# Kernel optimization log

Measured on AMD Instinct MI355X. Metric: run time of the kernel, lower is better.

The kernel has to match this reference:

```python
import jax, jax.numpy as jnp
import numpy as np

NEMBEDS = 512
EMBED_DIM = 64


def setup_inputs() -> dict:
    key = jax.random.key(0)
    k1, k2 = jax.random.split(key)
    z_e = jax.random.normal(k1, (32, EMBED_DIM, 64, 64), dtype=jnp.float32)
    codebook = jax.random.uniform(
        k2, (NEMBEDS, EMBED_DIM), dtype=jnp.float32,
        minval=-1.0 / NEMBEDS, maxval=1.0 / NEMBEDS)
    return {"z_e": z_e, "codebook": codebook}


def reference(z_e, codebook):
    # NCHW -> NHWC, flatten spatial+batch into tokens
    z = jnp.transpose(z_e, (0, 2, 3, 1))          # [B,H,W,D]
    B, H, W, D = z.shape
    flat = z.reshape(-1, D)                        # [N,D]
    # squared L2 distances (argmin of ||.||_2 == argmin of ||.||_2^2)
    # expanded form avoids the [N,K,D] broadcast intermediate
    d2 = (jnp.sum(flat * flat, axis=-1, keepdims=True)
          - 2.0 * flat @ codebook.T
          + jnp.sum(codebook * codebook, axis=-1))  # [N,K]
    inds = jnp.argmin(d2, axis=1)                   # [N]
    # direct gather == one-hot matmul lookup
    z_q = codebook[inds].reshape(B, H, W, D)        # [B,H,W,D]
    # commitment + codebook loss, per-batch mean over H,W,D
    sg = jax.lax.stop_gradient
    vq_loss = (jnp.mean((sg(z) - z_q) ** 2, axis=(1, 2, 3))
               + 0.25 * jnp.mean((z - sg(z_q)) ** 2, axis=(1, 2, 3)))  # [B]
    # straight-through estimator
    z_q_st = z + sg(z_q - z)
    out = jnp.transpose(z_q_st, (0, 3, 1, 2))       # back to NCHW
    return out, vq_loss, inds[:, None]
```

## Files before the change

kernel.cpp:

```cpp
#include <hip/hip_runtime.h>

#define NEMB 512
#define DIM 64
#define NB 32
#define HW 4096
#define NTOK (NB * HW)
#define TPB 512
#define TOKBLK 512
#define BLOCKS (NTOK / TOKBLK)

typedef float f32x16 __attribute__((ext_vector_type(16)));
typedef short bf16x8 __attribute__((ext_vector_type(8)));

__device__ __forceinline__ unsigned short f2bf(float f) {
    unsigned u = __float_as_uint(f);
    unsigned r = u + 0x7FFFu + ((u >> 16) & 1u);
    return (unsigned short)(r >> 16);
}
__device__ __forceinline__ float bf2f(unsigned short h) {
    return __uint_as_float((unsigned)h << 16);
}

__global__ void vq_prep(const float* __restrict__ cb, float* __restrict__ sumc)
{
    int k = blockIdx.x * 256 + threadIdx.x;
    if (k < NEMB) {
#pragma clang fp contract(off)
        float s = 0.f;
#pragma unroll
        for (int d = 0; d < DIM; ++d) {
            float v = cb[k * DIM + d];
            float p = v * v;
            s = s + p;
        }
        sumc[k] = s;
    }
}

__global__ __launch_bounds__(TPB, 4)
void vq_main(const float* __restrict__ z_e, const float* __restrict__ cb,
             const float* __restrict__ sumc, float* __restrict__ out,
             float* __restrict__ loss_part, float* __restrict__ inds_out)
{
    __shared__ uint4 ch_s[NEMB * 9];
    __shared__ float sumc_s[NEMB];
    __shared__ float red_s[TPB];

    const int tid  = threadIdx.x;
    const int gid  = blockIdx.x;
    const int b    = gid >> 3;
    const int base = (gid & 7) * TOKBLK;
    const int w    = tid >> 6;
    const int l    = tid & 63;
    const int col  = l & 31;
    const int half = l >> 5;

    float cmax_l = 0.f;
    {
        const float4* cbg = (const float4*)cb;
#pragma unroll
        for (int i = 0; i < 8; ++i) {
            int idx = i * TPB + tid;
            int c = idx >> 3, bd = idx & 7;
            float4 v0 = cbg[idx * 2];
            float4 v1 = cbg[idx * 2 + 1];
            float vv[8] = {v0.x, v0.y, v0.z, v0.w, v1.x, v1.y, v1.z, v1.w};
            unsigned wd[4];
#pragma unroll
            for (int q = 0; q < 4; ++q) {
                cmax_l = fmaxf(cmax_l, fmaxf(fabsf(vv[2 * q]), fabsf(vv[2 * q + 1])));
                wd[q] = (unsigned)f2bf(vv[2 * q]) | ((unsigned)f2bf(vv[2 * q + 1]) << 16);
            }
            int slot = (bd + c) & 7;
            ch_s[c * 9 + slot] = make_uint4(wd[0], wd[1], wd[2], wd[3]);
        }
    }
    const float sc_v = sumc[tid];
    sumc_s[tid] = sc_v;

    const float* zb = z_e + (size_t)b * DIM * HW;
    const int t0 = base + w * 64;
    uint4 bzh[2][4], bzl[2][4];
    float l1p[2] = {0.f, 0.f}, szp[2] = {0.f, 0.f};
#pragma unroll
    for (int tt = 0; tt < 2; ++tt) {
        int tok = t0 + tt * 32 + col;
#pragma unroll
        for (int ks = 0; ks < 4; ++ks) {
            unsigned hh[8], ll[8];
#pragma unroll
            for (int j = 0; j < 8; ++j) {
                int d = 16 * ks + 8 * half + j;
                float v = zb[(size_t)d * HW + tok];
                l1p[tt] += fabsf(v);
                szp[tt] = fmaf(v, v, szp[tt]);
                unsigned short h = f2bf(v);
                unsigned short lo = f2bf(v - bf2f(h));
                hh[j] = h; ll[j] = lo;
            }
            bzh[tt][ks] = make_uint4(hh[0] | (hh[1] << 16), hh[2] | (hh[3] << 16),
                                     hh[4] | (hh[5] << 16), hh[6] | (hh[7] << 16));
            bzl[tt][ks] = make_uint4(ll[0] | (ll[1] << 16), ll[2] | (ll[3] << 16),
                                     ll[4] | (ll[5] << 16), ll[6] | (ll[7] << 16));
        }
    }
    float L1[2], SZ[2];
#pragma unroll
    for (int tt = 0; tt < 2; ++tt) {
        L1[tt] = l1p[tt] + __shfl_xor(l1p[tt], 32);
        SZ[tt] = szp[tt] + __shfl_xor(szp[tt], 32);
    }

    {
        float cm = cmax_l, sm = sc_v;
#pragma unroll
        for (int off = 32; off; off >>= 1) {
            cm = fmaxf(cm, __shfl_xor(cm, off));
            sm = fmaxf(sm, __shfl_xor(sm, off));
        }
        if (l == 0) { red_s[w] = cm; red_s[8 + w] = sm; }
    }
    __syncthreads();
    float cmax = red_s[0], scmax = red_s[8];
#pragma unroll
    for (int i = 1; i < 8; ++i) {
        cmax  = fmaxf(cmax,  red_s[i]);
        scmax = fmaxf(scmax, red_s[8 + i]);
    }

    float gapd[2];
#pragma unroll
    for (int tt = 0; tt < 2; ++tt)
        gapd[tt] = 8.0e-3f * cmax * L1[tt] + 0.5f * scmax + 1.2e-7f * SZ[tt] + 1e-6f;

    unsigned mask0[8], mask1[8];
#pragma unroll
    for (int i = 0; i < 8; ++i) { mask0[i] = 0u; mask1[i] = 0u; }
    float runm[2] = {-3.402823466e38f, -3.402823466e38f};

    for (int ct = 0; ct < 16; ++ct) {
        bf16x8 ah[4];
        const int c = 32 * ct + col;
        const int rowb = c * 9;
#pragma unroll
        for (int ks = 0; ks < 4; ++ks) {
            int slot = ((2 * ks + half) + c) & 7;
            uint4 u1 = ch_s[rowb + slot];
            ah[ks] = *(bf16x8*)&u1;
        }
#pragma unroll
        for (int tt = 0; tt < 2; ++tt) {
            f32x16 acc = {0.f, 0.f, 0.f, 0.f, 0.f, 0.f, 0.f, 0.f,
                          0.f, 0.f, 0.f, 0.f, 0.f, 0.f, 0.f, 0.f};
#pragma unroll
            for (int ks = 0; ks < 4; ++ks)
                acc = __builtin_amdgcn_mfma_f32_32x32x16_bf16(ah[ks], *(bf16x8*)&bzh[tt][ks], acc, 0, 0, 0);
#pragma unroll
            for (int ks = 0; ks < 4; ++ks)
                acc = __builtin_amdgcn_mfma_f32_32x32x16_bf16(ah[ks], *(bf16x8*)&bzl[tt][ks], acc, 0, 0, 0);
            float m = acc[0];
#pragma unroll
            for (int r = 1; r < 16; ++r) m = fmaxf(m, acc[r]);
            float rm = fmaxf(tt == 0 ? runm[0] : runm[1], m);
            if (tt == 0) runm[0] = rm; else runm[1] = rm;
            float thr = rm - (tt == 0 ? gapd[0] : gapd[1]);
            unsigned bits = 0;
#pragma unroll
            for (int r = 0; r < 16; ++r)
                bits |= (acc[r] >= thr) ? (1u << r) : 0u;
            unsigned sh = bits << ((ct & 1) * 16);
            if (tt == 0) mask0[ct >> 1] |= sh; else mask1[ct >> 1] |= sh;
        }
    }

    unsigned om[8], xm[8];
#pragma unroll
    for (int i = 0; i < 8; ++i) {
        om[i] = half ? mask1[i] : mask0[i];
        xm[i] = __shfl_xor(half ? mask0[i] : mask1[i], 32);
    }

    const int hwme = base + tid;
    float z[DIM];
    float sumz;
    {
#pragma clang fp contract(off)
        sumz = 0.f;
#pragma unroll
        for (int d = 0; d < DIM; ++d) {
            float v = zb[(size_t)d * HW + hwme];
            z[d] = v;
            float p = v * v;
            sumz = sumz + p;
        }
    }

    float best = 3.402823466e38f;
    int bk = 0;
    for (int ct = 0; ct < 16; ++ct) {
        unsigned A = (om[ct >> 1] >> ((ct & 1) * 16)) & 0xFFFFu;
        unsigned B = (xm[ct >> 1] >> ((ct & 1) * 16)) & 0xFFFFu;
        unsigned wo = ((A & 0xFu)) | (((A >> 4) & 0xFu) << 8) |
                      (((A >> 8) & 0xFu) << 16) | (((A >> 12) & 0xFu) << 24);
        unsigned wx = ((B & 0xFu)) | (((B >> 4) & 0xFu) << 8) |
                      (((B >> 8) & 0xFu) << 16) | (((B >> 12) & 0xFu) << 24);
        unsigned wc = half ? ((wo << 4) | wx) : (wo | (wx << 4));
        while (wc) {
            int kk = __builtin_ctz(wc);
            wc &= wc - 1;
            int k = 32 * ct + kk;
            const float4* c4 = (const float4*)(cb + (size_t)k * DIM);
            float a0 = 0.f;
#pragma unroll
            for (int g = 0; g < DIM / 4; ++g) {
                float4 u = c4[g];
                a0 = fmaf(z[4 * g + 0], u.x, a0);
                a0 = fmaf(z[4 * g + 1], u.y, a0);
                a0 = fmaf(z[4 * g + 2], u.z, a0);
                a0 = fmaf(z[4 * g + 3], u.w, a0);
            }
            float d2 = (sumz - 2.0f * a0) + sumc_s[k];
            if (d2 < best) { best = d2; bk = k; }
        }
    }

    inds_out[(size_t)gid * TOKBLK + tid] = (float)bk;
    float* ob = out + (size_t)b * DIM * HW;
    float lsum = 0.f;
    const float4* q4 = (const float4*)(cb + (size_t)bk * DIM);
    {
#pragma clang fp contract(off)
#pragma unroll
        for (int g = 0; g < DIM / 4; ++g) {
            float4 qq = q4[g];
            float qv[4] = {qq.x, qq.y, qq.z, qq.w};
#pragma unroll
            for (int j = 0; j < 4; ++j) {
                int d = g * 4 + j;
                float t1 = qv[j] - z[d];
                ob[(size_t)d * HW + hwme] = z[d] + t1;
                float p = t1 * t1;
                lsum = lsum + p;
            }
        }
    }

    __syncthreads();
    red_s[tid] = lsum;
    __syncthreads();
#pragma unroll
    for (int s = 128; s > 0; s >>= 1) {
        if ((tid & 255) < s) red_s[tid] = red_s[tid] + red_s[tid + s];
        __syncthreads();
    }
    if (tid == 0)   loss_part[2 * gid]     = red_s[0];
    if (tid == 256) loss_part[2 * gid + 1] = red_s[256];
}

__global__ void vq_loss_final(const float* __restrict__ part,
                              float* __restrict__ loss_out)
{
    int b = threadIdx.x;
    if (b < NB) {
        float s = 0.f;
        for (int i = 0; i < 16; ++i)
            s = s + part[b * 16 + i];
        float m = s * (1.0f / (HW * DIM));
        loss_out[b] = m + 0.25f * m;
    }
}

extern "C" void kernel_launch(void* const* d_in, const int* in_sizes, int n_in,
                              void* d_out, int out_size, void* d_ws, size_t ws_size,
                              hipStream_t stream)
{
    const float* z_e = (const float*)d_in[0];
    const float* cb  = (const float*)d_in[1];

    float* out  = (float*)d_out;
    float* loss = out + (size_t)NB * DIM * HW;
    float* inds = loss + NB;

    float* part  = (float*)d_ws;
    float* sumcg = part + 512;

    vq_prep<<<2, 256, 0, stream>>>(cb, sumcg);
    vq_main<<<BLOCKS, TPB, 0, stream>>>(z_e, cb, sumcg, out, part, inds);
    vq_loss_final<<<1, 64, 0, stream>>>(part, loss);
}
```

Measured before the change: 100.6 us.

## Drop split-bf16 low part of z, fuse codebook norms into main kernel

Removes the low-order bf16 residual of z, which halves the MFMA count in the distance screening loop, and doubles the candidate gap margin to cover the extra rounding error. The codebook squared-norm prep kernel is folded into the main kernel, so each block recomputes the norms and one launch is removed. The padded 9-stride shared layout becomes 8-stride and relies on the existing XOR-style slot rotation to avoid bank conflicts. Risks are more candidates passing the wider threshold into the exact rescoring path, and redundant per-block norm work.

```diff
diff --git a/kernel.cpp b/kernel.cpp
--- a/kernel.cpp
+++ b/kernel.cpp
@@ -17,32 +17,13 @@
     unsigned r = u + 0x7FFFu + ((u >> 16) & 1u);
     return (unsigned short)(r >> 16);
 }
-__device__ __forceinline__ float bf2f(unsigned short h) {
-    return __uint_as_float((unsigned)h << 16);
-}
-
-__global__ void vq_prep(const float* __restrict__ cb, float* __restrict__ sumc)
-{
-    int k = blockIdx.x * 256 + threadIdx.x;
-    if (k < NEMB) {
-#pragma clang fp contract(off)
-        float s = 0.f;
-#pragma unroll
-        for (int d = 0; d < DIM; ++d) {
-            float v = cb[k * DIM + d];
-            float p = v * v;
-            s = s + p;
-        }
-        sumc[k] = s;
-    }
-}
 
 __global__ __launch_bounds__(TPB, 4)
 void vq_main(const float* __restrict__ z_e, const float* __restrict__ cb,
-             const float* __restrict__ sumc, float* __restrict__ out,
-             float* __restrict__ loss_part, float* __restrict__ inds_out)
+             float* __restrict__ out, float* __restrict__ loss_part,
+             float* __restrict__ inds_out)
 {
-    __shared__ uint4 ch_s[NEMB * 9];
+    __shared__ uint4 ch_s[NEMB * 8];
     __shared__ float sumc_s[NEMB];
     __shared__ float red_s[TPB];
 
@@ -72,36 +53,44 @@
                 wd[q] = (unsigned)f2bf(vv[2 * q]) | ((unsigned)f2bf(vv[2 * q + 1]) << 16);
             }
             int slot = (bd + c) & 7;
-            ch_s[c * 9 + slot] = make_uint4(wd[0], wd[1], wd[2], wd[3]);
-        }
-    }
-    const float sc_v = sumc[tid];
+            ch_s[c * 8 + slot] = make_uint4(wd[0], wd[1], wd[2], wd[3]);
+        }
+    }
+
+    float sc_v;
+    {
+#pragma clang fp contract(off)
+        float s = 0.f;
+#pragma unroll
+        for (int d = 0; d < DIM; ++d) {
+            float v = cb[tid * DIM + d];
+            float p = v * v;
+            s = s + p;
+        }
+        sc_v = s;
+    }
     sumc_s[tid] = sc_v;
 
     const float* zb = z_e + (size_t)b * DIM * HW;
     const int t0 = base + w * 64;
-    uint4 bzh[2][4], bzl[2][4];
+    uint4 bzh[2][4];
     float l1p[2] = {0.f, 0.f}, szp[2] = {0.f, 0.f};
 #pragma unroll
     for (int tt = 0; tt < 2; ++tt) {
         int tok = t0 + tt * 32 + col;
 #pragma unroll
         for (int ks = 0; ks < 4; ++ks) {
-            unsigned hh[8], ll[8];
+            unsigned hh[8];
 #pragma unroll
             for (int j = 0; j < 8; ++j) {
                 int d = 16 * ks + 8 * half + j;
                 float v = zb[(size_t)d * HW + tok];
                 l1p[tt] += fabsf(v);
                 szp[tt] = fmaf(v, v, szp[tt]);
-                unsigned short h = f2bf(v);
-                unsigned short lo = f2bf(v - bf2f(h));
-                hh[j] = h; ll[j] = lo;
+                hh[j] = f2bf(v);
             }
             bzh[tt][ks] = make_uint4(hh[0] | (hh[1] << 16), hh[2] | (hh[3] << 16),
                                      hh[4] | (hh[5] << 16), hh[6] | (hh[7] << 16));
-            bzl[tt][ks] = make_uint4(ll[0] | (ll[1] << 16), ll[2] | (ll[3] << 16),
-                                     ll[4] | (ll[5] << 16), ll[6] | (ll[7] << 16));
         }
     }
     float L1[2], SZ[2];
@@ -131,7 +120,7 @@
     float gapd[2];
 #pragma unroll
     for (int tt = 0; tt < 2; ++tt)
-        gapd[tt] = 8.0e-3f * cmax * L1[tt] + 0.5f * scmax + 1.2e-7f * SZ[tt] + 1e-6f;
+        gapd[tt] = 1.6e-2f * cmax * L1[tt] + 0.5f * scmax + 1.2e-7f * SZ[tt] + 1e-6f;
 
     unsigned mask0[8], mask1[8];
 #pragma unroll
@@ -141,7 +130,7 @@
     for (int ct = 0; ct < 16; ++ct) {
         bf16x8 ah[4];
         const int c = 32 * ct + col;
-        const int rowb = c * 9;
+        const int rowb = c * 8;
 #pragma unroll
         for (int ks = 0; ks < 4; ++ks) {
             int slot = ((2 * ks + half) + c) & 7;
@@ -155,9 +144,6 @@
 #pragma unroll
             for (int ks = 0; ks < 4; ++ks)
                 acc = __builtin_amdgcn_mfma_f32_32x32x16_bf16(ah[ks], *(bf16x8*)&bzh[tt][ks], acc, 0, 0, 0);
-#pragma unroll
-            for (int ks = 0; ks < 4; ++ks)
-                acc = __builtin_amdgcn_mfma_f32_32x32x16_bf16(ah[ks], *(bf16x8*)&bzl[tt][ks], acc, 0, 0, 0);
             float m = acc[0];
 #pragma unroll
             for (int r = 1; r < 16; ++r) m = fmaxf(m, acc[r]);
@@ -280,11 +266,8 @@
     float* out  = (float*)d_out;
     float* loss = out + (size_t)NB * DIM * HW;
     float* inds = loss + NB;
-
-    float* part  = (float*)d_ws;
-    float* sumcg = part + 512;
-
-    vq_prep<<<2, 256, 0, stream>>>(cb, sumcg);
-    vq_main<<<BLOCKS, TPB, 0, stream>>>(z_e, cb, sumcg, out, part, inds);
+    float* part = (float*)d_ws;
+
+    vq_main<<<BLOCKS, TPB, 0, stream>>>(z_e, cb, out, part, inds);
     vq_loss_final<<<1, 64, 0, stream>>>(part, loss);
 }
```

Result: faster. 93.55 us (-7.0%).
